# Performance work log

Hardware: AMD Instinct MI355X
Metric: run time of the kernel (lower is better)

The kernel has to match this reference:

```python
import jax, jax.numpy as jnp
import numpy as np

H, DM, LQ, LK, DK, DV = 16, 1024, 2048, 2048, 64, 64
B = 2

def setup_inputs() -> dict:
    key = jax.random.key(0)
    ks = jax.random.split(key, 12)
    s = 0.02  # init scale for weights
    return {
        "Q": jax.random.normal(ks[0], (B, LQ, DM), jnp.float32),
        "K": jax.random.normal(ks[1], (B, LK, DM), jnp.float32),
        "V": jax.random.normal(ks[2], (B, LK, DM), jnp.float32),
        "mask": jax.random.randint(ks[3], (B, LQ), 0, 2, jnp.int32),
        "W_Q": jax.random.normal(ks[4], (H * DK, DM), jnp.float32) * s,
        "b_Q": jnp.zeros((H * DK,), jnp.float32),
        "W_K": jax.random.normal(ks[5], (H * DK, DM), jnp.float32) * s,
        "b_K": jnp.zeros((H * DK,), jnp.float32),
        "W_V": jax.random.normal(ks[6], (H * DV, DM), jnp.float32) * s,
        "b_V": jnp.zeros((H * DV,), jnp.float32),
        "W_O": jax.random.normal(ks[7], (DM, H * DV), jnp.float32) * s,
        "b_O": jnp.zeros((DM,), jnp.float32),
    }

def reference(Q, K, V, mask, W_Q, b_Q, W_K, b_K, W_V, b_V, W_O, b_O):
    b = Q.shape[0]
    q = (Q @ W_Q.T + b_Q).reshape(b, LQ, H, DK)
    k = (K @ W_K.T + b_K).reshape(b, LK, H, DK)
    v = (V @ W_V.T + b_V).reshape(b, LK, H, DV)
    # scores: [b, h, q, k]
    A = jnp.einsum('bqhd,bkhd->bhqk', q, k) / jnp.sqrt(jnp.float32(DK))
    # mask masks whole QUERY rows; softmax is over the query axis (dim=1 in torch's [B*h, lq, lk])
    A = jnp.where(mask[:, None, :, None] == 0, -jnp.inf, A)
    alpha = jax.nn.softmax(A, axis=2)  # over query axis, per original masked branch
    out = jnp.einsum('bhqk,bkhd->bqhd', alpha, v).reshape(b, LQ, H * DV)
    return out @ W_O.T + b_O + Q  # output proj + residual
```

## Files before the change

### kernel.cpp

```cpp
#include <hip/hip_runtime.h>
#include <hip/hip_bf16.h>
#include <stdint.h>

using frag8 = __attribute__((ext_vector_type(8))) short;
using f32x4 = __attribute__((ext_vector_type(4))) float;

#define MFMA16 __builtin_amdgcn_mfma_f32_16x16x32_bf16

#if __has_builtin(__builtin_amdgcn_exp2f)
#define EXP2F(x) __builtin_amdgcn_exp2f(x)
#else
#define EXP2F(x) __expf((x) * 0.6931471805599453f)
#endif
#if __has_builtin(__builtin_amdgcn_rcpf)
#define RCPF(x) __builtin_amdgcn_rcpf(x)
#else
#define RCPF(x) (1.0f / (x))
#endif

#define SCALE_Q 0.18033688011112042f

__device__ __forceinline__ short f2bf(float f) {
    union { __hip_bfloat16 h; short s; } c;
    c.h = __float2bfloat16(f);
    return c.s;
}
__device__ __forceinline__ float bf2f(short s) {
    union { uint32_t u; float f; } x; x.u = ((uint32_t)(uint16_t)s) << 16;
    return x.f;
}
__device__ __forceinline__ uint32_t pack2bf(float a, float b) {
    float2 t; t.x = a; t.y = b;
    __hip_bfloat162 h = __float22bfloat162_rn(t);
    union { __hip_bfloat162 h; uint32_t u; } c; c.h = h;
    return c.u;
}
__device__ __forceinline__ uint32_t addpk(uint32_t a, uint32_t b) {
    float a0 = bf2f((short)(a & 0xffff)), a1 = bf2f((short)(a >> 16));
    float b0 = bf2f((short)(b & 0xffff)), b1 = bf2f((short)(b >> 16));
    return pack2bf(a0 + b0, a1 + b1);
}
__device__ __forceinline__ frag8 add8(uint4 x, uint4 y) {
    union { uint32_t u[4]; frag8 f; } r;
    r.u[0] = addpk(x.x, y.x); r.u[1] = addpk(x.y, y.y);
    r.u[2] = addpk(x.z, y.z); r.u[3] = addpk(x.w, y.w);
    return r.f;
}

__global__ __launch_bounds__(64) void k_compact(const int* __restrict__ mask,
                                                int* __restrict__ idx,
                                                int* __restrict__ invp,
                                                int* __restrict__ nU) {
    const int b = blockIdx.x, ln = threadIdx.x;
    const int* m = mask + b * 2048;
    int tot = 0;
    for (int c = 0; c < 32; c++)
        tot += __popcll(__ballot(m[c * 64 + ln] != 0));
    int base = 0, mbase = tot;
    for (int c = 0; c < 32; c++) {
        int i = c * 64 + ln;
        int mv = m[i];
        unsigned long long bal = __ballot(mv != 0);
        int rank = __popcll(bal & ((1ull << ln) - 1ull));
        int nb = __popcll(bal);
        int pos = mv ? (base + rank) : (mbase + ln - rank);
        invp[b * 2048 + i] = pos;
        if (mv) idx[b * 2048 + pos] = i;
        base += nb; mbase += 64 - nb;
    }
    if (ln == 0) nU[b] = tot;
}

__global__ __launch_bounds__(256) void k_zero2(uint4* __restrict__ a,
                                               uint4* __restrict__ b, int n16) {
    int i = blockIdx.x * 256 + threadIdx.x;
    if (i < n16) { uint4 z = {0, 0, 0, 0}; a[i] = z; b[i] = z; }
}

__global__ __launch_bounds__(256) void k_psum(short* __restrict__ p0,
                                              const short* __restrict__ p1, int n8) {
    int i = blockIdx.x * 256 + threadIdx.x;
    int st = gridDim.x * 256;
    for (; i < n8; i += st) {
        uint4 a = ((const uint4*)p0)[i];
        uint4 b = ((const uint4*)p1)[i];
        frag8 r = add8(a, b);
        ((uint4*)p0)[i] = *(uint4*)&r;
    }
}

__global__ __launch_bounds__(256) void k_cvt_all(
    const float* __restrict__ s0, const float* __restrict__ s1,
    const float* __restrict__ s2, const float* __restrict__ s3,
    const float* __restrict__ s4, const float* __restrict__ s5,
    const float* __restrict__ s6,
    short* __restrict__ d0, short* __restrict__ d1, short* __restrict__ d2,
    short* __restrict__ d3, short* __restrict__ d4, short* __restrict__ d5,
    short* __restrict__ d6) {
    const int A4 = 1048576, W4 = 262144;
    int i = blockIdx.x * 256 + threadIdx.x;
    int st = gridDim.x * 256;
    const int total = 3 * A4 + 4 * W4;
    for (; i < total; i += st) {
        const float* s; short* d; int j;
        if (i < A4)            { s = s0; d = d0; j = i; }
        else if (i < 2 * A4)   { s = s1; d = d1; j = i - A4; }
        else if (i < 3 * A4)   { s = s2; d = d2; j = i - 2 * A4; }
        else {
            int t = i - 3 * A4; int seg = t / W4; j = t - seg * W4;
            s = seg == 0 ? s3 : seg == 1 ? s4 : seg == 2 ? s5 : s6;
            d = seg == 0 ? d3 : seg == 1 ? d4 : seg == 2 ? d5 : d6;
        }
        float4 v = reinterpret_cast<const float4*>(s)[j];
        uint2 o;
        o.x = pack2bf(v.x, v.y);
        o.y = pack2bf(v.z, v.w);
        reinterpret_cast<uint2*>(d)[j] = o;
    }
}

__device__ __forceinline__ void stage64x128(const short* __restrict__ g, int rs,
                                            short* lds, int tid) {
#pragma unroll
    for (int j = 0; j < 2; j++) {
        int chunk = j * 256 + tid;
        int row = chunk >> 3, c = chunk & 7;
        int sc = c ^ (row & 7);
        __builtin_amdgcn_global_load_lds(
            (const __attribute__((address_space(1))) uint32_t*)(g + (size_t)row * rs + sc * 8),
            (__attribute__((address_space(3))) uint32_t*)(lds + (j * 256 + (tid & 192)) * 8),
            16, 0, 0);
    }
}
__device__ __forceinline__ frag8 ldswz(const short* lds, int row, int cc) {
    return *(const frag8*)(lds + row * 64 + ((cc ^ (row & 7)) << 3));
}

__device__ __forceinline__ void stage_gswz(const short* __restrict__ g,
                                           short* lds, int tid) {
#pragma unroll
    for (int j = 0; j < 2; j++) {
        int c = j * 256 + tid;
        int lrow = c >> 3;
        int sc = (c & 7) ^ (lrow & 7);
        int grow = lrow * 2 + (sc >> 2);
        int gcol = (sc & 3) * 8;
        __builtin_amdgcn_global_load_lds(
            (const __attribute__((address_space(1))) uint32_t*)(g + (size_t)grow * 1024 + gcol),
            (__attribute__((address_space(3))) uint32_t*)(lds + (j * 256 + (tid & 192)) * 8),
            16, 0, 0);
    }
}
__device__ __forceinline__ void stage_gswz64(const short* __restrict__ g,
                                             short* lds, int tid) {
    int c = tid;
    int lrow = c >> 3;
    int sc = (c & 7) ^ (lrow & 7);
    int grow = lrow * 2 + (sc >> 2);
    int gcol = (sc & 3) * 8;
    __builtin_amdgcn_global_load_lds(
        (const __attribute__((address_space(1))) uint32_t*)(g + (size_t)grow * 1024 + gcol),
        (__attribute__((address_space(3))) uint32_t*)(lds + (tid & 192) * 8),
        16, 0, 0);
}
__device__ __forceinline__ frag8 ldgswz(const short* lds, int row, int cc) {
    int lrow = row >> 1;
    int s = (((row & 1) << 2) + cc) ^ (lrow & 7);
    return *(const frag8*)(lds + lrow * 64 + s * 8);
}

__global__ __launch_bounds__(256) void k_proj3(
    const short* __restrict__ A0, const short* __restrict__ A1, const short* __restrict__ A2,
    const short* __restrict__ B0, const short* __restrict__ B1, const short* __restrict__ B2,
    const float* __restrict__ bias0, const float* __restrict__ bias1, const float* __restrict__ bias2,
    const int* __restrict__ invp,
    short* __restrict__ dst0, short* __restrict__ dst1, short* __restrict__ dst2) {
    __shared__ short lA[2][4096];
    __shared__ short lB[2][4096];
    const int wg = blockIdx.x;
    const int tmlow = wg & 7, tnb = (wg >> 3) & 7, rest = wg >> 6;
    const int tmh = rest & 3, z = rest >> 2;
    const int tmb = tmlow | (tmh << 3);
    const short* A  = z == 0 ? A0 : z == 1 ? A1 : A2;
    const short* Bt = z == 0 ? B0 : z == 1 ? B1 : B2;
    const float* bias = z == 0 ? bias0 : z == 1 ? bias1 : bias2;
    short* dst = z == 0 ? dst0 : z == 1 ? dst1 : dst2;
    const float scale = z == 0 ? SCALE_Q : 1.0f;

    const int tid = threadIdx.x, w = tid >> 6, ln = tid & 63;
    const int wm = w >> 1, wn = w & 1, r16 = ln & 15, g = ln >> 4;
    const int tn = tnb * 128, tm = tmb * 128;
    const short* Ab = A + (size_t)tm * 1024;
    const short* Bb = Bt + (size_t)tn * 1024;

    f32x4 acc[4][4] = {};
    stage_gswz(Ab, &lA[0][0], tid);
    stage_gswz(Bb, &lB[0][0], tid);
    int buf = 0;
    for (int ks = 0; ks < 32; ks++) {
        __syncthreads();
        if (ks + 1 < 32) {
            stage_gswz(Ab + (ks + 1) * 32, &lA[buf ^ 1][0], tid);
            stage_gswz(Bb + (ks + 1) * 32, &lB[buf ^ 1][0], tid);
        }
        frag8 af[4], bg[4];
#pragma unroll
        for (int mf = 0; mf < 4; mf++)
            af[mf] = ldgswz(&lA[buf][0], wm * 64 + mf * 16 + r16, g);
#pragma unroll
        for (int nf = 0; nf < 4; nf++)
            bg[nf] = ldgswz(&lB[buf][0], wn * 64 + nf * 16 + r16, g);
#pragma unroll
        for (int mf = 0; mf < 4; mf++)
#pragma unroll
            for (int nf = 0; nf < 4; nf++)
                acc[mf][nf] = MFMA16(af[mf], bg[nf], acc[mf][nf], 0, 0, 0);
        buf ^= 1;
    }
#pragma unroll
    for (int mf = 0; mf < 4; mf++)
#pragma unroll
        for (int r = 0; r < 4; r++) {
            int m = tm + wm * 64 + mf * 16 + g * 4 + r;
            int b = m >> 11, seq = m & 2047;
            int sq = (z == 0) ? invp[b * 2048 + seq] : seq;
#pragma unroll
            for (int nf = 0; nf < 4; nf++) {
                int n = tn + wn * 64 + nf * 16 + r16;
                float val = (acc[mf][nf][r] + bias[n]) * scale;
                int h = n >> 6, d = n & 63;
                dst[((size_t)(b * 16 + h) * 2048 + sq) * 64 + d] = f2bf(val);
            }
        }
}

__global__ __launch_bounds__(256, 3) void k_stats(const short* __restrict__ k_s,
                                                  const short* __restrict__ q_s,
                                                  const int* __restrict__ nU,
                                                  const short* __restrict__ v_s,
                                                  short* __restrict__ vhatT) {
    __shared__ short lQ[2][4096];
    __shared__ float lD[128];
    __shared__ short lT[128 * 70];
    const int wg = blockIdx.x;
    const int x = wg & 7, r2 = wg >> 3;
    const int kt = r2 & 15;
    const int bh = x + 8 * (r2 >> 4);
    const int b = bh >> 4;
    const int n = nU[b], nUr = (n + 63) & ~63;
    const int tid = threadIdx.x, w = tid >> 6, ln = tid & 63;
    const int r16 = ln & 15, g = ln >> 4;
    const int kbase = kt * 128 + w * 32;

    const short* kp = k_s + ((size_t)bh * 2048 + kbase) * 64;
    frag8 kf[2][2];
#pragma unroll
    for (int mfk = 0; mfk < 2; mfk++)
#pragma unroll
        for (int kk = 0; kk < 2; kk++)
            kf[mfk][kk] = *(const frag8*)(kp + (mfk * 16 + r16) * 64 + kk * 32 + g * 8);

    const short* qsp = q_s + (size_t)bh * 2048 * 64;
    float dacc[2][4] = {};
    const f32x4 z4 = {0.f, 0.f, 0.f, 0.f};

    if (nUr > 0) {
        stage64x128(qsp, 64, &lQ[0][0], tid);
        int buf = 0;
        for (int qb = 0; qb < nUr; qb += 64) {
            __syncthreads();
            if (qb + 64 < nUr)
                stage64x128(qsp + (size_t)(qb + 64) * 64, 64, &lQ[buf ^ 1][0], tid);
            const short* Qc = &lQ[buf][0];
#pragma unroll
            for (int nf = 0; nf < 4; nf++) {
                float fm = (qb + nf * 16 + r16 < n) ? 1.0f : 0.0f;
                frag8 bq0 = ldswz(Qc, nf * 16 + r16, g);
                frag8 bq1 = ldswz(Qc, nf * 16 + r16, 4 + g);
#pragma unroll
                for (int mfk = 0; mfk < 2; mfk++) {
                    f32x4 s = MFMA16(kf[mfk][0], bq0, z4, 0, 0, 0);
                    s = MFMA16(kf[mfk][1], bq1, s, 0, 0, 0);
#pragma unroll
                    for (int r = 0; r < 4; r++)
                        dacc[mfk][r] += fm * EXP2F(s[r]);
                }
            }
            buf ^= 1;
        }
    }
#pragma unroll
    for (int mfk = 0; mfk < 2; mfk++)
#pragma unroll
        for (int r = 0; r < 4; r++) {
            float v = dacc[mfk][r];
#pragma unroll
            for (int off = 1; off < 16; off <<= 1)
                v += __shfl_xor(v, off, 16);
            dacc[mfk][r] = v;
        }
    if (r16 == 0) {
#pragma unroll
        for (int mfk = 0; mfk < 2; mfk++)
#pragma unroll
            for (int r = 0; r < 4; r++)
                lD[w * 32 + mfk * 16 + g * 4 + r] = RCPF(dacc[mfk][r]);
    }
    const short* vrow = v_s + ((size_t)bh * 2048 + kt * 128) * 64;
#pragma unroll
    for (int i = 0; i < 8; i++) {
        int idx4 = i * 256 + tid;
        int row = idx4 >> 4, c4 = idx4 & 15;
        uint2 u = *(const uint2*)(vrow + (size_t)row * 64 + c4 * 4);
        *(uint32_t*)&lT[row * 70 + c4 * 4]     = u.x;
        *(uint32_t*)&lT[row * 70 + c4 * 4 + 2] = u.y;
    }
    __syncthreads();
    {
        int d = tid >> 2, kc = tid & 3;
        short* dstp = vhatT + ((size_t)bh * 64 + d) * 2048 + kt * 128 + kc * 32;
        uint32_t wd[16];
#pragma unroll
        for (int j2 = 0; j2 < 16; j2++) {
            int k0 = kc * 32 + j2 * 2;
            float v0 = bf2f(lT[k0 * 70 + d]) * lD[k0];
            float v1 = bf2f(lT[(k0 + 1) * 70 + d]) * lD[k0 + 1];
            wd[j2] = pack2bf(v0, v1);
        }
#pragma unroll
        for (int j4 = 0; j4 < 4; j4++) {
            uint4 o = {wd[j4 * 4], wd[j4 * 4 + 1], wd[j4 * 4 + 2], wd[j4 * 4 + 3]};
            *((uint4*)dstp + j4) = o;
        }
    }
}

__global__ __launch_bounds__(256, 3) void k_apply(const short* __restrict__ q_s,
                                                  const short* __restrict__ k_s,
                                                  const short* __restrict__ vhatT,
                                                  const int* __restrict__ idx,
                                                  const int* __restrict__ nU,
                                                  short* __restrict__ p0,
                                                  short* __restrict__ p1) {
    __shared__ short lK[2][4096];
    __shared__ short lV[2][4096];
    __shared__ short lP[128 * 64];
    const int wg = blockIdx.x;
    const int x = wg & 7, r2 = wg >> 3;
    const int qt = r2 & 15, y = r2 >> 4;
    const int bhsp = (y << 3) | x;
    const int bh = bhsp >> 1, sp = bhsp & 1;
    const int b = bh >> 4, h = bh & 15;
    const int n = nU[b];
    if (qt * 128 >= n) return;
    const int tid = threadIdx.x, w = tid >> 6, ln = tid & 63;
    const int r16 = ln & 15, g = ln >> 4;

    const short* qp = q_s + ((size_t)bh * 2048 + qt * 128 + w * 32) * 64;
    frag8 qf[2][2];
#pragma unroll
    for (int qi = 0; qi < 2; qi++)
#pragma unroll
        for (int kk = 0; kk < 2; kk++)
            qf[qi][kk] = *(const frag8*)(qp + (qi * 16 + r16) * 64 + kk * 32 + g * 8);

    const short* kp = k_s + ((size_t)bh * 2048 + sp * 1024) * 64;
    const short* vp = vhatT + (size_t)bh * 64 * 2048 + sp * 1024;

    f32x4 oacc[2][4] = {};
    const f32x4 z4 = {0.f, 0.f, 0.f, 0.f};

    stage64x128(kp, 64, &lK[0][0], tid);
    stage64x128(vp, 2048, &lV[0][0], tid);
    int buf = 0;
    for (int kb = 0; kb < 1024; kb += 64) {
        __syncthreads();
        if (kb + 64 < 1024) {
            stage64x128(kp + (size_t)(kb + 64) * 64, 64, &lK[buf ^ 1][0], tid);
            stage64x128(vp + kb + 64, 2048, &lV[buf ^ 1][0], tid);
        }
        const short* Kc = &lK[buf][0];
        const short* Vc = &lV[buf][0];
        frag8 vb[4][2];
#pragma unroll
        for (int nf = 0; nf < 4; nf++)
#pragma unroll
            for (int kk = 0; kk < 2; kk++)
                vb[nf][kk] = ldswz(Vc, nf * 16 + r16, kk * 4 + g);
#pragma unroll
        for (int qi = 0; qi < 2; qi++) {
            const int prow = w * 32 + qi * 16 + r16;
            const int rx = prow & 7;
#pragma unroll
            for (int mf2 = 0; mf2 < 4; mf2++) {
                f32x4 s = z4;
#pragma unroll
                for (int kk = 0; kk < 2; kk++)
                    s = MFMA16(ldswz(Kc, mf2 * 16 + r16, kk * 4 + g), qf[qi][kk], s, 0, 0, 0);
                float e0 = EXP2F(s[0]), e1 = EXP2F(s[1]);
                float e2 = EXP2F(s[2]), e3 = EXP2F(s[3]);
                uint2 pk;
                pk.x = pack2bf(e0, e1);
                pk.y = pack2bf(e2, e3);
                int o = mf2 * 32 + g * 8;
                int addr = prow * 128 + (((o >> 4) ^ rx) << 4) + (o & 15);
                *(uint2*)((char*)lP + addr) = pk;
            }
        }
#pragma unroll
        for (int qi = 0; qi < 2; qi++) {
            const int prow = w * 32 + qi * 16 + r16;
            const int rx = prow & 7;
            frag8 pa[2];
#pragma unroll
            for (int kk = 0; kk < 2; kk++)
                pa[kk] = *(const frag8*)((char*)lP + prow * 128 + (((kk * 4 + g) ^ rx) << 4));
#pragma unroll
            for (int nf = 0; nf < 4; nf++)
#pragma unroll
                for (int kk = 0; kk < 2; kk++)
                    oacc[qi][nf] = MFMA16(pa[kk], vb[nf][kk], oacc[qi][nf], 0, 0, 0);
        }
        buf ^= 1;
    }
    short* op = sp ? p1 : p0;
#pragma unroll
    for (int qi = 0; qi < 2; qi++)
#pragma unroll
        for (int r = 0; r < 4; r++) {
            int lq = qt * 128 + w * 32 + qi * 16 + g * 4 + r;
            if (lq < n) {
                int qg = idx[b * 2048 + lq];
#pragma unroll
                for (int nf = 0; nf < 4; nf++) {
                    int d = nf * 16 + r16;
                    op[((size_t)(b * 2048 + qg)) * 1024 + h * 64 + d] = f2bf(oacc[qi][nf][r]);
                }
            }
        }
}

__global__ __launch_bounds__(256) void k_final(const short* __restrict__ A,
                                               const short* __restrict__ Bt,
                                               const float* __restrict__ bias,
                                               const float* __restrict__ Qres,
                                               float* __restrict__ out) {
    __shared__ short lA[2][4096];
    __shared__ short lB[2][2048];
    const int wg = blockIdx.x;
    const int x = wg & 7, r2 = wg >> 3;
    const int tnb = r2 & 15, tmh = r2 >> 4;
    const int tmb = x | (tmh << 3);
    const int tid = threadIdx.x, w = tid >> 6, ln = tid & 63;
    const int wm = w >> 1, wn = w & 1, r16 = ln & 15, g = ln >> 4;
    const int tn = tnb * 64, tm = tmb * 128;
    const short* Ab = A + (size_t)tm * 1024;
    const short* Bb = Bt + (size_t)tn * 1024;

    f32x4 acc[4][2] = {};
    stage_gswz(Ab, &lA[0][0], tid);
    stage_gswz64(Bb, &lB[0][0], tid);
    int buf = 0;
    for (int ks = 0; ks < 32; ks++) {
        __syncthreads();
        if (ks + 1 < 32) {
            stage_gswz(Ab + (ks + 1) * 32, &lA[buf ^ 1][0], tid);
            stage_gswz64(Bb + (ks + 1) * 32, &lB[buf ^ 1][0], tid);
        }
        frag8 af[4], bg[2];
#pragma unroll
        for (int mf = 0; mf < 4; mf++)
            af[mf] = ldgswz(&lA[buf][0], wm * 64 + mf * 16 + r16, g);
#pragma unroll
        for (int nf = 0; nf < 2; nf++)
            bg[nf] = ldgswz(&lB[buf][0], wn * 32 + nf * 16 + r16, g);
#pragma unroll
        for (int mf = 0; mf < 4; mf++)
#pragma unroll
            for (int nf = 0; nf < 2; nf++)
                acc[mf][nf] = MFMA16(af[mf], bg[nf], acc[mf][nf], 0, 0, 0);
        buf ^= 1;
    }
#pragma unroll
    for (int mf = 0; mf < 4; mf++)
#pragma unroll
        for (int nf = 0; nf < 2; nf++)
#pragma unroll
            for (int r = 0; r < 4; r++) {
                int m = tm + wm * 64 + mf * 16 + g * 4 + r;
                int n = tn + wn * 32 + nf * 16 + r16;
                float val = acc[mf][nf][r] + bias[n] + Qres[(size_t)m * 1024 + n];
                out[(size_t)m * 1024 + n] = val;
            }
}

extern "C" void kernel_launch(void* const* d_in, const int* in_sizes, int n_in,
                              void* d_out, int out_size, void* d_ws, size_t ws_size,
                              hipStream_t stream) {
    (void)in_sizes; (void)n_in; (void)out_size; (void)ws_size;
    const float* Qf  = (const float*)d_in[0];
    const float* Kf  = (const float*)d_in[1];
    const float* Vf  = (const float*)d_in[2];
    const int*   msk = (const int*)d_in[3];
    const float* WQ  = (const float*)d_in[4];
    const float* bQ  = (const float*)d_in[5];
    const float* WK  = (const float*)d_in[6];
    const float* bK  = (const float*)d_in[7];
    const float* WV  = (const float*)d_in[8];
    const float* bV  = (const float*)d_in[9];
    const float* WO  = (const float*)d_in[10];
    const float* bO  = (const float*)d_in[11];
    float* out = (float*)d_out;

    char* p = (char*)d_ws;
    const size_t SZ_ACT = (size_t)4096 * 1024 * 2;
    const size_t SZ_W   = (size_t)1024 * 1024 * 2;
    short* Qb  = (short*)p; p += SZ_ACT;
    short* Kb  = (short*)p; p += SZ_ACT;
    short* Vb  = (short*)p; p += SZ_ACT;
    short* q_s = (short*)p; p += SZ_ACT;
    short* k_s = (short*)p; p += SZ_ACT;
    short* v_s = (short*)p; p += SZ_ACT;
    short* Wqb = (short*)p; p += SZ_W;
    short* Wkb = (short*)p; p += SZ_W;
    short* Wvb = (short*)p; p += SZ_W;
    short* Wob = (short*)p; p += SZ_W;
    int* idx  = (int*)p; p += (size_t)2 * 2048 * 4;
    int* invp = (int*)p; p += (size_t)2 * 2048 * 4;
    int* nU   = (int*)p; p += 256;
    short* vhatT = Qb;
    short* p0    = Kb;
    short* p1    = Vb;

    k_compact<<<2, 64, 0, stream>>>(msk, idx, invp, nU);

    k_cvt_all<<<4096, 256, 0, stream>>>(Qf, Kf, Vf, WQ, WK, WV, WO,
                                        Qb, Kb, Vb, Wqb, Wkb, Wvb, Wob);

    k_proj3<<<768, 256, 0, stream>>>(Qb, Kb, Vb, Wqb, Wkb, Wvb,
                                     bQ, bK, bV, invp, q_s, k_s, v_s);

    k_stats<<<512, 256, 0, stream>>>(k_s, q_s, nU, v_s, vhatT);

    k_zero2<<<2048, 256, 0, stream>>>((uint4*)p0, (uint4*)p1, 524288);

    k_apply<<<1024, 256, 0, stream>>>(q_s, k_s, vhatT, idx, nU, p0, p1);

    k_psum<<<2048, 256, 0, stream>>>(p0, p1, 524288);

    k_final<<<512, 256, 0, stream>>>(p0, Wob, bO, Qf, out);
}
```

Measured before the change: 157.9 us.

## Keep attention output compacted; skip masked rows in Q projection and output GEMM

Q rows are permuted into compacted order during bf16 conversion. The Q projection and the output projection then skip tiles made entirely of masked rows. The attention output stays in compacted row order, so the zeroing kernel is removed, and the final GEMM scatters rows back through idx. A separate kernel writes Q+bias for masked rows. This saves GEMM work for masked queries and one memset, at the cost of an extra elementwise pass and scattered output writes.

Result: no change. 155.3 us (-1.7%).

```diff
diff --git a/kernel.cpp b/kernel.cpp
--- a/kernel.cpp
+++ b/kernel.cpp
@@ -71,12 +71,6 @@
     if (ln == 0) nU[b] = tot;
 }
 
-__global__ __launch_bounds__(256) void k_zero2(uint4* __restrict__ a,
-                                               uint4* __restrict__ b, int n16) {
-    int i = blockIdx.x * 256 + threadIdx.x;
-    if (i < n16) { uint4 z = {0, 0, 0, 0}; a[i] = z; b[i] = z; }
-}
-
 __global__ __launch_bounds__(256) void k_psum(short* __restrict__ p0,
                                               const short* __restrict__ p1, int n8) {
     int i = blockIdx.x * 256 + threadIdx.x;
@@ -89,11 +83,30 @@
     }
 }
 
+__global__ __launch_bounds__(256) void k_maskout(const int* __restrict__ mask,
+                                                 const float* __restrict__ bO,
+                                                 const float* __restrict__ Qf,
+                                                 float* __restrict__ out) {
+    int i = blockIdx.x * 256 + threadIdx.x;
+    int st = gridDim.x * 256;
+    const int total = 4096 * 256;
+    for (; i < total; i += st) {
+        int row = i >> 8, c4 = i & 255;
+        if (mask[row] == 0) {
+            float4 q = ((const float4*)Qf)[i];
+            float4 bv = ((const float4*)bO)[c4];
+            float4 o; o.x = q.x + bv.x; o.y = q.y + bv.y;
+            o.z = q.z + bv.z; o.w = q.w + bv.w;
+            ((float4*)out)[i] = o;
+        }
+    }
+}
+
 __global__ __launch_bounds__(256) void k_cvt_all(
     const float* __restrict__ s0, const float* __restrict__ s1,
     const float* __restrict__ s2, const float* __restrict__ s3,
     const float* __restrict__ s4, const float* __restrict__ s5,
-    const float* __restrict__ s6,
+    const float* __restrict__ s6, const int* __restrict__ invp,
     short* __restrict__ d0, short* __restrict__ d1, short* __restrict__ d2,
     short* __restrict__ d3, short* __restrict__ d4, short* __restrict__ d5,
     short* __restrict__ d6) {
@@ -103,7 +116,8 @@
     const int total = 3 * A4 + 4 * W4;
     for (; i < total; i += st) {
         const float* s; short* d; int j;
-        if (i < A4)            { s = s0; d = d0; j = i; }
+        bool permQ = false;
+        if (i < A4)            { s = s0; d = d0; j = i; permQ = true; }
         else if (i < 2 * A4)   { s = s1; d = d1; j = i - A4; }
         else if (i < 3 * A4)   { s = s2; d = d2; j = i - 2 * A4; }
         else {
@@ -115,7 +129,13 @@
         uint2 o;
         o.x = pack2bf(v.x, v.y);
         o.y = pack2bf(v.z, v.w);
-        reinterpret_cast<uint2*>(d)[j] = o;
+        int jd = j;
+        if (permQ) {
+            int row = j >> 8, c4 = j & 255;
+            int nrow = (row & ~2047) + invp[row];
+            jd = (nrow << 8) + c4;
+        }
+        reinterpret_cast<uint2*>(d)[jd] = o;
     }
 }
 
@@ -173,7 +193,7 @@
     const short* __restrict__ A0, const short* __restrict__ A1, const short* __restrict__ A2,
     const short* __restrict__ B0, const short* __restrict__ B1, const short* __restrict__ B2,
     const float* __restrict__ bias0, const float* __restrict__ bias1, const float* __restrict__ bias2,
-    const int* __restrict__ invp,
+    const int* __restrict__ nU,
     short* __restrict__ dst0, short* __restrict__ dst1, short* __restrict__ dst2) {
     __shared__ short lA[2][4096];
     __shared__ short lB[2][4096];
@@ -181,6 +201,7 @@
     const int tmlow = wg & 7, tnb = (wg >> 3) & 7, rest = wg >> 6;
     const int tmh = rest & 3, z = rest >> 2;
     const int tmb = tmlow | (tmh << 3);
+    if (z == 0 && (tmb & 15) * 128 >= nU[tmb >> 4]) return;
     const short* A  = z == 0 ? A0 : z == 1 ? A1 : A2;
     const short* Bt = z == 0 ? B0 : z == 1 ? B1 : B2;
     const float* bias = z == 0 ? bias0 : z == 1 ? bias1 : bias2;
@@ -223,13 +244,12 @@
         for (int r = 0; r < 4; r++) {
             int m = tm + wm * 64 + mf * 16 + g * 4 + r;
             int b = m >> 11, seq = m & 2047;
-            int sq = (z == 0) ? invp[b * 2048 + seq] : seq;
 #pragma unroll
             for (int nf = 0; nf < 4; nf++) {
                 int n = tn + wn * 64 + nf * 16 + r16;
                 float val = (acc[mf][nf][r] + bias[n]) * scale;
                 int h = n >> 6, d = n & 63;
-                dst[((size_t)(b * 16 + h) * 2048 + sq) * 64 + d] = f2bf(val);
+                dst[((size_t)(b * 16 + h) * 2048 + seq) * 64 + d] = f2bf(val);
             }
         }
 }
@@ -338,7 +358,6 @@
 __global__ __launch_bounds__(256, 3) void k_apply(const short* __restrict__ q_s,
                                                   const short* __restrict__ k_s,
                                                   const short* __restrict__ vhatT,
-                                                  const int* __restrict__ idx,
                                                   const int* __restrict__ nU,
                                                   short* __restrict__ p0,
                                                   short* __restrict__ p1) {
@@ -430,11 +449,10 @@
         for (int r = 0; r < 4; r++) {
             int lq = qt * 128 + w * 32 + qi * 16 + g * 4 + r;
             if (lq < n) {
-                int qg = idx[b * 2048 + lq];
 #pragma unroll
                 for (int nf = 0; nf < 4; nf++) {
                     int d = nf * 16 + r16;
-                    op[((size_t)(b * 2048 + qg)) * 1024 + h * 64 + d] = f2bf(oacc[qi][nf][r]);
+                    op[((size_t)(b * 2048 + lq)) * 1024 + h * 64 + d] = f2bf(oacc[qi][nf][r]);
                 }
             }
         }
@@ -444,6 +462,8 @@
                                                const short* __restrict__ Bt,
                                                const float* __restrict__ bias,
                                                const float* __restrict__ Qres,
+                                               const int* __restrict__ idx,
+                                               const int* __restrict__ nU,
                                                float* __restrict__ out) {
     __shared__ short lA[2][4096];
     __shared__ short lB[2][2048];
@@ -451,6 +471,9 @@
     const int x = wg & 7, r2 = wg >> 3;
     const int tnb = r2 & 15, tmh = r2 >> 4;
     const int tmb = x | (tmh << 3);
+    const int bb = tmb >> 4;
+    const int n = nU[bb];
+    if ((tmb & 15) * 128 >= n) return;
     const int tid = threadIdx.x, w = tid >> 6, ln = tid & 63;
     const int wm = w >> 1, wn = w & 1, r16 = ln & 15, g = ln >> 4;
     const int tn = tnb * 64, tm = tmb * 128;
@@ -484,14 +507,20 @@
 #pragma unroll
     for (int mf = 0; mf < 4; mf++)
 #pragma unroll
-        for (int nf = 0; nf < 2; nf++)
-#pragma unroll
-            for (int r = 0; r < 4; r++) {
-                int m = tm + wm * 64 + mf * 16 + g * 4 + r;
-                int n = tn + wn * 32 + nf * 16 + r16;
-                float val = acc[mf][nf][r] + bias[n] + Qres[(size_t)m * 1024 + n];
-                out[(size_t)m * 1024 + n] = val;
+        for (int r = 0; r < 4; r++) {
+            int m = tm + wm * 64 + mf * 16 + g * 4 + r;
+            int i = m & 2047;
+            if (i < n) {
+                int qg = idx[bb * 2048 + i];
+                size_t rowo = ((size_t)(bb * 2048 + qg)) * 1024;
+#pragma unroll
+                for (int nf = 0; nf < 2; nf++) {
+                    int nn = tn + wn * 32 + nf * 16 + r16;
+                    float val = acc[mf][nf][r] + bias[nn] + Qres[rowo + nn];
+                    out[rowo + nn] = val;
+                }
             }
+        }
 }
 
 extern "C" void kernel_launch(void* const* d_in, const int* in_sizes, int n_in,
@@ -534,19 +563,19 @@
 
     k_compact<<<2, 64, 0, stream>>>(msk, idx, invp, nU);
 
-    k_cvt_all<<<4096, 256, 0, stream>>>(Qf, Kf, Vf, WQ, WK, WV, WO,
+    k_cvt_all<<<4096, 256, 0, stream>>>(Qf, Kf, Vf, WQ, WK, WV, WO, invp,
                                         Qb, Kb, Vb, Wqb, Wkb, Wvb, Wob);
 
     k_proj3<<<768, 256, 0, stream>>>(Qb, Kb, Vb, Wqb, Wkb, Wvb,
-                                     bQ, bK, bV, invp, q_s, k_s, v_s);
+                                     bQ, bK, bV, nU, q_s, k_s, v_s);
 
     k_stats<<<512, 256, 0, stream>>>(k_s, q_s, nU, v_s, vhatT);
 
-    k_zero2<<<2048, 256, 0, stream>>>((uint4*)p0, (uint4*)p1, 524288);
-
-    k_apply<<<1024, 256, 0, stream>>>(q_s, k_s, vhatT, idx, nU, p0, p1);
+    k_apply<<<1024, 256, 0, stream>>>(q_s, k_s, vhatT, nU, p0, p1);
 
     k_psum<<<2048, 256, 0, stream>>>(p0, p1, 524288);
 
-    k_final<<<512, 256, 0, stream>>>(p0, Wob, bO, Qf, out);
-}
+    k_maskout<<<2048, 256, 0, stream>>>(msk, bO, Qf, out);
+
+    k_final<<<512, 256, 0, stream>>>(p0, Wob, bO, Qf, idx, nU, out);
+}
```
